# Optimization experiments

Hardware: AMD Instinct MI355X
Metric: run time of the kernel (lower is better)

## Reference

```python
import jax, jax.numpy as jnp
import numpy as np

NUM_QUBITS = 6
NUM_LAYER = 3
INPUT_SIZE = 512
NUM_ANGLES = NUM_LAYER * (4 * NUM_QUBITS - 1)  # 69
BATCH = 65536


def _apply_1q(state, U, wire):
    # state: [B, 2,2,2,2,2,2]; U: [B,2,2] complex
    axis = 1 + wire
    s = jnp.moveaxis(state, axis, -1)
    shp = s.shape
    s = s.reshape(s.shape[0], -1, 2)
    s = jnp.einsum('bij,bkj->bki', U, s)
    return jnp.moveaxis(s.reshape(shp), -1, axis)


def _apply_2q(state, U, w0, w1):
    # state: [B, 2,...,2]; U: [B,4,4] complex; wires (w0,w1) with w0 the high bit
    s = jnp.moveaxis(state, (1 + w0, 1 + w1), (-2, -1))
    shp = s.shape
    s = s.reshape(s.shape[0], -1, 4)
    s = jnp.einsum('bij,bkj->bki', U, s)
    return jnp.moveaxis(s.reshape(shp), (-2, -1), (1 + w0, 1 + w1))


def _rxx_mat(theta):
    c = jnp.cos(theta / 2).astype(jnp.complex64)
    s = (-1j * jnp.sin(theta / 2)).astype(jnp.complex64)
    z = jnp.zeros_like(c)
    return jnp.stack([
        jnp.stack([c, z, z, s], -1),
        jnp.stack([z, c, s, z], -1),
        jnp.stack([z, s, c, z], -1),
        jnp.stack([s, z, z, c], -1),
    ], -2)


def _u3_mat(theta, phi, lam):
    # standard U3 gate: [B,2,2]
    ct = jnp.cos(theta / 2).astype(jnp.complex64)
    st = jnp.sin(theta / 2).astype(jnp.complex64)
    e = lambda a: jnp.exp(1j * a.astype(jnp.complex64))
    return jnp.stack([
        jnp.stack([ct, -e(lam) * st], -1),
        jnp.stack([e(phi) * st, e(phi + lam) * ct], -1),
    ], -2)


def _circuit(angles):
    B = angles.shape[0]
    n = NUM_QUBITS
    state = jnp.zeros((B, 2 ** n), jnp.complex64).at[:, 0].set(1.0)
    state = state.reshape((B,) + (2,) * n)
    per_layer = 4 * n - 1
    for lay in range(NUM_LAYER):
        a = angles[:, lay * per_layer:(lay + 1) * per_layer]
        k = 0
        for i in range(n - 1):
            state = _apply_2q(state, _rxx_mat(a[:, k]), i, i + 1)
            k += 1
            state = _apply_1q(state, _u3_mat(a[:, k], a[:, k + 1], a[:, k + 2]), i)
            k += 3
        state = _apply_1q(state, _u3_mat(a[:, k], a[:, k + 1], a[:, k + 2]), n - 1)
    state = state.reshape(B, 2 ** n)
    # return real/imag stacked: [B, 2, 2^n] float32
    return jnp.stack([state.real, state.imag], axis=1).astype(jnp.float32)


def setup_inputs() -> dict:
    key = jax.random.key(0)
    kx, kw, kb = jax.random.split(key, 3)
    x = jax.random.normal(kx, (BATCH, INPUT_SIZE), dtype=jnp.float32)
    W = jax.random.normal(kw, (NUM_ANGLES, INPUT_SIZE), dtype=jnp.float32) / np.sqrt(INPUT_SIZE)
    b = jax.random.normal(kb, (NUM_ANGLES,), dtype=jnp.float32) * 0.01
    return {"x": x, "W": W, "b": b}


def reference(x, W, b):
    angles = x @ W.T + b  # [B, 69]
    return _circuit(angles)
```

## Files before the change

### kernel.cpp

```cpp
#include <hip/hip_runtime.h>

#define NA    69
#define KDIM  512
#define BM    128
#define BK    64
#define GT    256
#define ASTRIDE 132
#define CROWS 256
#define BLK   256
#define LSTRIDE 33

typedef __attribute__((ext_vector_type(8))) short short8v;
typedef __attribute__((ext_vector_type(4))) float f32x4;
typedef __attribute__((ext_vector_type(4))) unsigned short us4;

__device__ __forceinline__ unsigned short bf16_rne(float x) {
    unsigned u = __float_as_uint(x);
    unsigned r = u + 0x7FFF + ((u >> 16) & 1);
    return (unsigned short)(r >> 16);
}

__global__ void w_convert(const float* __restrict__ W,
                          unsigned short* __restrict__ Whf,
                          unsigned short* __restrict__ Wlf)
{
    int tid = blockIdx.x * 256 + threadIdx.x;
    if (tid >= 16 * 5 * 64) return;
    int ksg = tid / 320;
    int rem = tid % 320;
    int nt  = rem / 64;
    int l   = rem % 64;
    int n   = nt * 16 + (l & 15);
    int k   = ksg * 32 + (l >> 4) * 8;
#pragma unroll
    for (int j = 0; j < 8; ++j) {
        float w = (n < NA) ? W[(size_t)n * KDIM + k + j] : 0.f;
        unsigned short h = bf16_rne(w);
        float hf = __uint_as_float((unsigned)h << 16);
        Whf[(size_t)tid * 8 + j] = h;
        Wlf[(size_t)tid * 8 + j] = bf16_rne(w - hf);
    }
}


template<int M0, int M1>
__device__ __forceinline__ void rxx_l(float* sr, float* si, float th) {
    float h = 0.5f * th, c, sn;
    __sincosf(h, &sn, &c);
    constexpr int M = M0 | M1;
#pragma unroll
    for (int j = 0; j < 32; ++j) {
        if (j & M0) continue;
        const int p = j ^ M;
        float ar = sr[j], ai = si[j], br = sr[p], bi = si[p];
        sr[j] = c * ar + sn * bi;
        si[j] = c * ai - sn * br;
        sr[p] = c * br + sn * ai;
        si[p] = c * bi - sn * ar;
    }
}

template<int M>
__device__ __forceinline__ void u3_l(float* sr, float* si,
                                     float th, float ph, float la) {
    float h = 0.5f * th;
    float ct, st, cph, sph, cla, sla;
    __sincosf(h,  &st,  &ct);
    __sincosf(ph, &sph, &cph);
    __sincosf(la, &sla, &cla);
    float cpl = cph * cla - sph * sla;
    float spl = sph * cla + cph * sla;
    float m01r = -cla * st, m01i = -sla * st;
    float m10r =  cph * st, m10i =  sph * st;
    float m11r =  cpl * ct, m11i =  spl * ct;
#pragma unroll
    for (int j = 0; j < 32; ++j) {
        if (j & M) continue;
        const int p = j | M;
        float ar = sr[j], ai = si[j], br = sr[p], bi = si[p];
        sr[j] = ct * ar + m01r * br - m01i * bi;
        si[j] = ct * ai + m01r * bi + m01i * br;
        sr[p] = m10r * ar - m10i * ai + m11r * br - m11i * bi;
        si[p] = m10r * ai + m10i * ar + m11r * bi + m11i * br;
    }
}

__device__ __forceinline__ void rxx01_x(float* sr, float* si, float th) {
    float h = 0.5f * th, c, sn;
    __sincosf(h, &sn, &c);
#pragma unroll
    for (int j = 0; j < 16; ++j) {
        const int p = j + 16;
        float crj = __shfl_xor(sr[p], 32), cij = __shfl_xor(si[p], 32);
        float crp = __shfl_xor(sr[j], 32), cip = __shfl_xor(si[j], 32);
        float aj = sr[j], bj = si[j], ap = sr[p], bp = si[p];
        sr[j] = c * aj + sn * cij;  si[j] = c * bj - sn * crj;
        sr[p] = c * ap + sn * cip;  si[p] = c * bp - sn * crp;
    }
}

__device__ __forceinline__ void u30_x(float* sr, float* si, int par,
                                      float th, float ph, float la) {
    float h = 0.5f * th;
    float ct, st, cph, sph, cla, sla;
    __sincosf(h,  &st,  &ct);
    __sincosf(ph, &sph, &cph);
    __sincosf(la, &sla, &cla);
    float cpl = cph * cla - sph * sla;
    float spl = sph * cla + cph * sla;
    float m01r = -cla * st, m01i = -sla * st;
    float m10r =  cph * st, m10i =  sph * st;
    float m11r =  cpl * ct, m11i =  spl * ct;
    float Ar = par ? m11r : ct,   Ai = par ? m11i : 0.f;
    float Br = par ? m10r : m01r, Bi = par ? m10i : m01i;
#pragma unroll
    for (int j = 0; j < 32; ++j) {
        float cr = __shfl_xor(sr[j], 32), ci = __shfl_xor(si[j], 32);
        float a = sr[j], bb = si[j];
        sr[j] = Ar * a  - Ai * bb + Br * cr - Bi * ci;
        si[j] = Ar * bb + Ai * a  + Br * ci + Bi * cr;
    }
}


__global__ __launch_bounds__(GT, 3) void qrnn_fused3(
    const float* __restrict__ x,
    const unsigned short* __restrict__ Whf, const unsigned short* __restrict__ Wlf,
    const float* __restrict__ b, float* __restrict__ out)
{
    __shared__ __align__(16) char smem[53248];
    unsigned short* Ah = (unsigned short*)smem;
    unsigned short* Al = (unsigned short*)(smem + 16384);
    unsigned short* Bh = (unsigned short*)(smem + 32768);
    unsigned short* Bl = (unsigned short*)(smem + 43008);
    float* as_ = (float*)smem;

    const int t    = threadIdx.x;
    const int lane = t & 63;
    const int wave = t >> 6;
    const int mb   = blockIdx.x * BM;

    f32x4 acc[2][5];
#pragma unroll
    for (int mt = 0; mt < 2; ++mt)
#pragma unroll
        for (int nt = 0; nt < 5; ++nt) acc[mt][nt] = (f32x4){0.f, 0.f, 0.f, 0.f};

    float4 vA[8];
    short8v vBh0, vBl0, vBh1, vBl1, vBh2, vBl2;

#pragma unroll
    for (int q = 0; q < 8; ++q) {
        int f = t + q * GT, row = f >> 4, col4 = f & 15;
        vA[q] = *reinterpret_cast<const float4*>(
            &x[(size_t)(mb + row) * KDIM + col4 * 4]);
    }
    vBh0 = *reinterpret_cast<const short8v*>(Whf + t * 8);
    vBl0 = *reinterpret_cast<const short8v*>(Wlf + t * 8);
    vBh1 = *reinterpret_cast<const short8v*>(Whf + (t + 256) * 8);
    vBl1 = *reinterpret_cast<const short8v*>(Wlf + (t + 256) * 8);
    if (t < 128) {
        vBh2 = *reinterpret_cast<const short8v*>(Whf + (t + 512) * 8);
        vBl2 = *reinterpret_cast<const short8v*>(Wlf + (t + 512) * 8);
    }

#pragma unroll
    for (int c = 0; c < KDIM / BK; ++c) {
#pragma unroll
        for (int q = 0; q < 8; ++q) {
            int f = t + q * GT, row = f >> 4, col4 = f & 15;
            float vals[4] = {vA[q].x, vA[q].y, vA[q].z, vA[q].w};
            us4 h, lo;
#pragma unroll
            for (int j = 0; j < 4; ++j) {
                unsigned u = __float_as_uint(vals[j]);
                h[j] = (unsigned short)(u >> 16);
                float hf = __uint_as_float(u & 0xFFFF0000u);
                lo[j] = bf16_rne(vals[j] - hf);
            }
            int sw   = (col4 >> 1) ^ (row & 7);
            int byte = row * (BK * 2) + sw * 16 + (col4 & 1) * 8;
            *reinterpret_cast<us4*>((char*)Ah + byte) = h;
            *reinterpret_cast<us4*>((char*)Al + byte) = lo;
        }
        *reinterpret_cast<short8v*>(Bh + t * 8) = vBh0;
        *reinterpret_cast<short8v*>(Bl + t * 8) = vBl0;
        *reinterpret_cast<short8v*>(Bh + (t + 256) * 8) = vBh1;
        *reinterpret_cast<short8v*>(Bl + (t + 256) * 8) = vBl1;
        if (t < 128) {
            *reinterpret_cast<short8v*>(Bh + (t + 512) * 8) = vBh2;
            *reinterpret_cast<short8v*>(Bl + (t + 512) * 8) = vBl2;
        }
        if (c + 1 < KDIM / BK) {
#pragma unroll
            for (int q = 0; q < 8; ++q) {
                int f = t + q * GT, row = f >> 4, col4 = f & 15;
                vA[q] = *reinterpret_cast<const float4*>(
                    &x[(size_t)(mb + row) * KDIM + (c + 1) * BK + col4 * 4]);
            }
            size_t base = (size_t)(c + 1) * 5120;
            vBh0 = *reinterpret_cast<const short8v*>(Whf + base + t * 8);
            vBl0 = *reinterpret_cast<const short8v*>(Wlf + base + t * 8);
            vBh1 = *reinterpret_cast<const short8v*>(Whf + base + (t + 256) * 8);
            vBl1 = *reinterpret_cast<const short8v*>(Wlf + base + (t + 256) * 8);
            if (t < 128) {
                vBh2 = *reinterpret_cast<const short8v*>(Whf + base + (t + 512) * 8);
                vBl2 = *reinterpret_cast<const short8v*>(Wlf + base + (t + 512) * 8);
            }
        }
        __syncthreads();

#pragma unroll
        for (int ks = 0; ks < BK / 32; ++ks) {
            short8v ah[2], al[2];
#pragma unroll
            for (int mt = 0; mt < 2; ++mt) {
                int row = wave * 32 + mt * 16 + (lane & 15);
                int c8  = ks * 4 + (lane >> 4);
                int sw  = c8 ^ (row & 7);
                int abyte = row * (BK * 2) + sw * 16;
                ah[mt] = *reinterpret_cast<const short8v*>((char*)Ah + abyte);
                al[mt] = *reinterpret_cast<const short8v*>((char*)Al + abyte);
            }
#pragma unroll
            for (int nt = 0; nt < 5; ++nt) {
                int boff = ((ks * 5 + nt) * 64 + lane) * 8;
                short8v bh = *reinterpret_cast<const short8v*>(Bh + boff);
                short8v bl = *reinterpret_cast<const short8v*>(Bl + boff);
#pragma unroll
                for (int mt = 0; mt < 2; ++mt) {
                    acc[mt][nt] = __builtin_amdgcn_mfma_f32_16x16x32_bf16(ah[mt], bh, acc[mt][nt], 0, 0, 0);
                    acc[mt][nt] = __builtin_amdgcn_mfma_f32_16x16x32_bf16(al[mt], bh, acc[mt][nt], 0, 0, 0);
                    acc[mt][nt] = __builtin_amdgcn_mfma_f32_16x16x32_bf16(ah[mt], bl, acc[mt][nt], 0, 0, 0);
                }
            }
        }
        __syncthreads();
    }

#pragma unroll
    for (int mt = 0; mt < 2; ++mt)
#pragma unroll
        for (int nt = 0; nt < 5; ++nt) {
            int n = nt * 16 + (lane & 15);
            if (n < NA) {
                float bias = b[n];
                int m = wave * 32 + mt * 16 + (lane >> 4) * 4;
                f32x4 v = acc[mt][nt];
#pragma unroll
                for (int j = 0; j < 4; ++j)
                    as_[n * ASTRIDE + m + j] = v[j] + bias;
            }
        }
    __syncthreads();

    const int par = lane >> 5;
    const int rl  = (lane & 31) + wave * 32;

    float sr[32], si[32];
#pragma unroll
    for (int j = 0; j < 32; ++j) { sr[j] = 0.f; si[j] = 0.f; }
    if (par == 0) sr[0] = 1.f;

#define ANG(i) as_[(i) * ASTRIDE + rl]
#pragma unroll 1
    for (int lay = 0; lay < 3; ++lay) {
        const int base = lay * 23;
        rxx01_x(sr, si, ANG(base + 0));
        u30_x  (sr, si, par, ANG(base + 1), ANG(base + 2), ANG(base + 3));
        rxx_l<16, 8>(sr, si, ANG(base + 4));
        u3_l<16>(sr, si, ANG(base + 5),  ANG(base + 6),  ANG(base + 7));
        rxx_l<8, 4>(sr, si, ANG(base + 8));
        u3_l<8>(sr, si, ANG(base + 9),  ANG(base + 10), ANG(base + 11));
        rxx_l<4, 2>(sr, si, ANG(base + 12));
        u3_l<4>(sr, si, ANG(base + 13), ANG(base + 14), ANG(base + 15));
        rxx_l<2, 1>(sr, si, ANG(base + 16));
        u3_l<2>(sr, si, ANG(base + 17), ANG(base + 18), ANG(base + 19));
        u3_l<1>(sr, si, ANG(base + 20), ANG(base + 21), ANG(base + 22));
    }
#undef ANG

    float* o = out + (size_t)(mb + rl) * 128 + par * 32;
#pragma unroll
    for (int q = 0; q < 8; ++q)
        *reinterpret_cast<float4*>(&o[q * 4]) =
            make_float4(sr[q*4], sr[q*4+1], sr[q*4+2], sr[q*4+3]);
#pragma unroll
    for (int q = 0; q < 8; ++q)
        *reinterpret_cast<float4*>(&o[64 + q * 4]) =
            make_float4(si[q*4], si[q*4+1], si[q*4+2], si[q*4+3]);
}


__global__ __launch_bounds__(BLK, 1) void angles_gemm(
    const float* __restrict__ x, const float* __restrict__ W,
    const float* __restrict__ b, float* __restrict__ ang,
    int row_base, int pass_rows)
{
    const int t     = threadIdx.x;
    const int lrow0 = blockIdx.x * BLK;
    __shared__ float xs[BLK * LSTRIDE];
    float acc[NA];
#pragma unroll
    for (int a = 0; a < NA; ++a) acc[a] = b[a];
    for (int kc = 0; kc < KDIM; kc += 32) {
        __syncthreads();
#pragma unroll
        for (int it = 0; it < 8; ++it) {
            int f4 = it * BLK + t;
            int r  = f4 >> 3;
            int kq = f4 & 7;
            float4 v = *reinterpret_cast<const float4*>(
                &x[(size_t)(row_base + lrow0 + r) * KDIM + kc + kq * 4]);
            *reinterpret_cast<float4*>(&xs[r * LSTRIDE + kq * 4]) = v;
        }
        __syncthreads();
        float4 xv[8];
#pragma unroll
        for (int q = 0; q < 8; ++q)
            xv[q] = *reinterpret_cast<const float4*>(&xs[t * LSTRIDE + q * 4]);
#pragma unroll
        for (int a = 0; a < NA; ++a) {
            const float* wa = W + a * KDIM + kc;
            float s = 0.f;
#pragma unroll
            for (int q = 0; q < 8; ++q) {
                s += xv[q].x * wa[q * 4 + 0];
                s += xv[q].y * wa[q * 4 + 1];
                s += xv[q].z * wa[q * 4 + 2];
                s += xv[q].w * wa[q * 4 + 3];
            }
            acc[a] += s;
        }
    }
    const int lrow = lrow0 + t;
#pragma unroll
    for (int a = 0; a < NA; ++a)
        ang[(size_t)a * pass_rows + lrow] = acc[a];
}

__global__ __launch_bounds__(512, 2) void circuit2g(
    const float* __restrict__ ang, float* __restrict__ out,
    int stride, int row_base)
{
    const int t    = threadIdx.x;
    const int lane = t & 63;
    const int wv   = t >> 6;
    const int par  = lane >> 5;
    const int rl   = (lane & 31) + wv * 32;
    const int row0 = blockIdx.x * CROWS;

    __shared__ float as_[NA][CROWS];
    for (int i = t; i < NA * CROWS; i += 512) {
        int a = i >> 8, r = i & 255;
        as_[a][r] = ang[(size_t)a * stride + row0 + r];
    }
    __syncthreads();

    float sr[32], si[32];
#pragma unroll
    for (int j = 0; j < 32; ++j) { sr[j] = 0.f; si[j] = 0.f; }
    if (par == 0) sr[0] = 1.f;

#define ANG(i) as_[(i)][rl]
#pragma unroll 1
    for (int lay = 0; lay < 3; ++lay) {
        const int base = lay * 23;
        rxx01_x(sr, si, ANG(base + 0));
        u30_x  (sr, si, par, ANG(base + 1), ANG(base + 2), ANG(base + 3));
        rxx_l<16, 8>(sr, si, ANG(base + 4));
        u3_l<16>(sr, si, ANG(base + 5),  ANG(base + 6),  ANG(base + 7));
        rxx_l<8, 4>(sr, si, ANG(base + 8));
        u3_l<8>(sr, si, ANG(base + 9),  ANG(base + 10), ANG(base + 11));
        rxx_l<4, 2>(sr, si, ANG(base + 12));
        u3_l<4>(sr, si, ANG(base + 13), ANG(base + 14), ANG(base + 15));
        rxx_l<2, 1>(sr, si, ANG(base + 16));
        u3_l<2>(sr, si, ANG(base + 17), ANG(base + 18), ANG(base + 19));
        u3_l<1>(sr, si, ANG(base + 20), ANG(base + 21), ANG(base + 22));
    }
#undef ANG

    float* o = out + (size_t)(row_base + row0 + rl) * 128 + par * 32;
#pragma unroll
    for (int q = 0; q < 8; ++q)
        *reinterpret_cast<float4*>(&o[q * 4]) =
            make_float4(sr[q*4], sr[q*4+1], sr[q*4+2], sr[q*4+3]);
#pragma unroll
    for (int q = 0; q < 8; ++q)
        *reinterpret_cast<float4*>(&o[64 + q * 4]) =
            make_float4(si[q*4], si[q*4+1], si[q*4+2], si[q*4+3]);
}


extern "C" void kernel_launch(void* const* d_in, const int* in_sizes, int n_in,
                              void* d_out, int out_size, void* d_ws, size_t ws_size,
                              hipStream_t stream) {
    const float* x = (const float*)d_in[0];
    const float* W = (const float*)d_in[1];
    const float* b = (const float*)d_in[2];
    float* out = (float*)d_out;
    const int batch = in_sizes[0] / KDIM;

    const size_t wf_elems = (size_t)16 * 5 * 64 * 8;
    const size_t need     = 2 * wf_elems * 2;

    if (ws_size >= need && (batch % BM) == 0) {
        unsigned short* Whf = (unsigned short*)d_ws;
        unsigned short* Wlf = Whf + wf_elems;
        hipLaunchKernelGGL(w_convert, dim3((16 * 5 * 64 + 255) / 256), dim3(256),
                           0, stream, W, Whf, Wlf);
        hipLaunchKernelGGL(qrnn_fused3, dim3(batch / BM), dim3(GT), 0, stream,
                           x, Whf, Wlf, b, out);
        return;
    }

    float* ws = (float*)d_ws;
    size_t max_rows = ws_size / ((size_t)NA * sizeof(float));
    int rows_per_pass = (int)((max_rows / CROWS) * CROWS);
    if (rows_per_pass > batch) rows_per_pass = batch;
    if (rows_per_pass < CROWS) return;
    for (int r0 = 0; r0 < batch; r0 += rows_per_pass) {
        int pr = batch - r0;
        if (pr > rows_per_pass) pr = rows_per_pass;
        hipLaunchKernelGGL(angles_gemm, dim3(pr / BLK), dim3(BLK), 0, stream,
                           x, W, b, ws, r0, pr);
        hipLaunchKernelGGL(circuit2g, dim3(pr / CROWS), dim3(512), 0, stream,
                           ws, out, pr, r0);
    }
}
```

Before: 65.65 us.

## Halve fused GEMM+circuit row tile to 64 and raise occupancy

The fused kernel now processes 64 rows per block instead of 128, with one MFMA row tile per wave instead of two. This shrinks LDS use and register pressure and raises launch bounds to 4 blocks per CU, giving twice as many blocks. The cost is that only two of the four waves run the circuit simulation, so half the threads sit idle in that phase. Each W fragment is also reloaded per 64 rows rather than per 128, doubling B traffic.

Result: slower. 138.5 us (+110.9%).

```diff
diff --git a/kernel.cpp b/kernel.cpp
--- a/kernel.cpp
+++ b/kernel.cpp
@@ -2,10 +2,10 @@
 
 #define NA    69
 #define KDIM  512
-#define BM    128
+#define BM    64
 #define BK    64
 #define GT    256
-#define ASTRIDE 132
+#define ASTR  68
 #define CROWS 256
 #define BLK   256
 #define LSTRIDE 33
@@ -44,7 +44,7 @@
 
 
 template<int M0, int M1>
-__device__ __forceinline__ void rxx_l(float* sr, float* si, float th) {
+__device__ __forceinline__ void rxx_l32(float* sr, float* si, float th) {
     float h = 0.5f * th, c, sn;
     __sincosf(h, &sn, &c);
     constexpr int M = M0 | M1;
@@ -61,8 +61,8 @@
 }
 
 template<int M>
-__device__ __forceinline__ void u3_l(float* sr, float* si,
-                                     float th, float ph, float la) {
+__device__ __forceinline__ void u3_l32(float* sr, float* si,
+                                       float th, float ph, float la) {
     float h = 0.5f * th;
     float ct, st, cph, sph, cla, sla;
     __sincosf(h,  &st,  &ct);
@@ -85,7 +85,7 @@
     }
 }
 
-__device__ __forceinline__ void rxx01_x(float* sr, float* si, float th) {
+__device__ __forceinline__ void rxx01_x32(float* sr, float* si, float th) {
     float h = 0.5f * th, c, sn;
     __sincosf(h, &sn, &c);
 #pragma unroll
@@ -99,8 +99,8 @@
     }
 }
 
-__device__ __forceinline__ void u30_x(float* sr, float* si, int par,
-                                      float th, float ph, float la) {
+__device__ __forceinline__ void u30_x32(float* sr, float* si, int par,
+                                        float th, float ph, float la) {
     float h = 0.5f * th;
     float ct, st, cph, sph, cla, sla;
     __sincosf(h,  &st,  &ct);
@@ -123,16 +123,16 @@
 }
 
 
-__global__ __launch_bounds__(GT, 3) void qrnn_fused3(
+__global__ __launch_bounds__(GT, 4) void qrnn_fused5(
     const float* __restrict__ x,
     const unsigned short* __restrict__ Whf, const unsigned short* __restrict__ Wlf,
     const float* __restrict__ b, float* __restrict__ out)
 {
-    __shared__ __align__(16) char smem[53248];
+    __shared__ __align__(16) char smem[36864];
     unsigned short* Ah = (unsigned short*)smem;
-    unsigned short* Al = (unsigned short*)(smem + 16384);
-    unsigned short* Bh = (unsigned short*)(smem + 32768);
-    unsigned short* Bl = (unsigned short*)(smem + 43008);
+    unsigned short* Al = (unsigned short*)(smem + 8192);
+    unsigned short* Bh = (unsigned short*)(smem + 16384);
+    unsigned short* Bl = (unsigned short*)(smem + 26624);
     float* as_ = (float*)smem;
 
     const int t    = threadIdx.x;
@@ -140,17 +140,15 @@
     const int wave = t >> 6;
     const int mb   = blockIdx.x * BM;
 
-    f32x4 acc[2][5];
-#pragma unroll
-    for (int mt = 0; mt < 2; ++mt)
-#pragma unroll
-        for (int nt = 0; nt < 5; ++nt) acc[mt][nt] = (f32x4){0.f, 0.f, 0.f, 0.f};
-
-    float4 vA[8];
+    f32x4 acc[5];
+#pragma unroll
+    for (int nt = 0; nt < 5; ++nt) acc[nt] = (f32x4){0.f, 0.f, 0.f, 0.f};
+
+    float4 vA[4];
     short8v vBh0, vBl0, vBh1, vBl1, vBh2, vBl2;
 
 #pragma unroll
-    for (int q = 0; q < 8; ++q) {
+    for (int q = 0; q < 4; ++q) {
         int f = t + q * GT, row = f >> 4, col4 = f & 15;
         vA[q] = *reinterpret_cast<const float4*>(
             &x[(size_t)(mb + row) * KDIM + col4 * 4]);
@@ -167,7 +165,7 @@
 #pragma unroll
     for (int c = 0; c < KDIM / BK; ++c) {
 #pragma unroll
-        for (int q = 0; q < 8; ++q) {
+        for (int q = 0; q < 4; ++q) {
             int f = t + q * GT, row = f >> 4, col4 = f & 15;
             float vals[4] = {vA[q].x, vA[q].y, vA[q].z, vA[q].w};
             us4 h, lo;
@@ -193,7 +191,7 @@
         }
         if (c + 1 < KDIM / BK) {
 #pragma unroll
-            for (int q = 0; q < 8; ++q) {
+            for (int q = 0; q < 4; ++q) {
                 int f = t + q * GT, row = f >> 4, col4 = f & 15;
                 vA[q] = *reinterpret_cast<const float4*>(
                     &x[(size_t)(mb + row) * KDIM + (c + 1) * BK + col4 * 4]);
@@ -212,83 +210,76 @@
 
 #pragma unroll
         for (int ks = 0; ks < BK / 32; ++ks) {
-            short8v ah[2], al[2];
-#pragma unroll
-            for (int mt = 0; mt < 2; ++mt) {
-                int row = wave * 32 + mt * 16 + (lane & 15);
-                int c8  = ks * 4 + (lane >> 4);
-                int sw  = c8 ^ (row & 7);
-                int abyte = row * (BK * 2) + sw * 16;
-                ah[mt] = *reinterpret_cast<const short8v*>((char*)Ah + abyte);
-                al[mt] = *reinterpret_cast<const short8v*>((char*)Al + abyte);
-            }
+            int row = wave * 16 + (lane & 15);
+            int c8  = ks * 4 + (lane >> 4);
+            int sw  = c8 ^ (row & 7);
+            int abyte = row * (BK * 2) + sw * 16;
+            short8v ah = *reinterpret_cast<const short8v*>((char*)Ah + abyte);
+            short8v al = *reinterpret_cast<const short8v*>((char*)Al + abyte);
 #pragma unroll
             for (int nt = 0; nt < 5; ++nt) {
                 int boff = ((ks * 5 + nt) * 64 + lane) * 8;
                 short8v bh = *reinterpret_cast<const short8v*>(Bh + boff);
                 short8v bl = *reinterpret_cast<const short8v*>(Bl + boff);
-#pragma unroll
-                for (int mt = 0; mt < 2; ++mt) {
-                    acc[mt][nt] = __builtin_amdgcn_mfma_f32_16x16x32_bf16(ah[mt], bh, acc[mt][nt], 0, 0, 0);
-                    acc[mt][nt] = __builtin_amdgcn_mfma_f32_16x16x32_bf16(al[mt], bh, acc[mt][nt], 0, 0, 0);
-                    acc[mt][nt] = __builtin_amdgcn_mfma_f32_16x16x32_bf16(ah[mt], bl, acc[mt][nt], 0, 0, 0);
-                }
+                acc[nt] = __builtin_amdgcn_mfma_f32_16x16x32_bf16(ah, bh, acc[nt], 0, 0, 0);
+                acc[nt] = __builtin_amdgcn_mfma_f32_16x16x32_bf16(al, bh, acc[nt], 0, 0, 0);
+                acc[nt] = __builtin_amdgcn_mfma_f32_16x16x32_bf16(ah, bl, acc[nt], 0, 0, 0);
             }
         }
         __syncthreads();
     }
 
 #pragma unroll
-    for (int mt = 0; mt < 2; ++mt)
-#pragma unroll
-        for (int nt = 0; nt < 5; ++nt) {
-            int n = nt * 16 + (lane & 15);
-            if (n < NA) {
-                float bias = b[n];
-                int m = wave * 32 + mt * 16 + (lane >> 4) * 4;
-                f32x4 v = acc[mt][nt];
-#pragma unroll
-                for (int j = 0; j < 4; ++j)
-                    as_[n * ASTRIDE + m + j] = v[j] + bias;
-            }
-        }
+    for (int nt = 0; nt < 5; ++nt) {
+        int n = nt * 16 + (lane & 15);
+        if (n < NA) {
+            float bias = b[n];
+            int m0 = wave * 16 + (lane >> 4) * 4;
+            f32x4 v = acc[nt];
+            float4 o = make_float4(v[0] + bias, v[1] + bias,
+                                   v[2] + bias, v[3] + bias);
+            *reinterpret_cast<float4*>(&as_[n * ASTR + m0]) = o;
+        }
+    }
     __syncthreads();
 
-    const int par = lane >> 5;
-    const int rl  = (lane & 31) + wave * 32;
-
-    float sr[32], si[32];
-#pragma unroll
-    for (int j = 0; j < 32; ++j) { sr[j] = 0.f; si[j] = 0.f; }
-    if (par == 0) sr[0] = 1.f;
-
-#define ANG(i) as_[(i) * ASTRIDE + rl]
+    if (wave < 2) {
+        const int par = lane >> 5;
+        const int rl  = (lane & 31) + wave * 32;
+
+        float sr[32], si[32];
+#pragma unroll
+        for (int j = 0; j < 32; ++j) { sr[j] = 0.f; si[j] = 0.f; }
+        if (par == 0) sr[0] = 1.f;
+
+#define ANG(i) as_[(i) * ASTR + rl]
 #pragma unroll 1
-    for (int lay = 0; lay < 3; ++lay) {
-        const int base = lay * 23;
-        rxx01_x(sr, si, ANG(base + 0));
-        u30_x  (sr, si, par, ANG(base + 1), ANG(base + 2), ANG(base + 3));
-        rxx_l<16, 8>(sr, si, ANG(base + 4));
-        u3_l<16>(sr, si, ANG(base + 5),  ANG(base + 6),  ANG(base + 7));
-        rxx_l<8, 4>(sr, si, ANG(base + 8));
-        u3_l<8>(sr, si, ANG(base + 9),  ANG(base + 10), ANG(base + 11));
-        rxx_l<4, 2>(sr, si, ANG(base + 12));
-        u3_l<4>(sr, si, ANG(base + 13), ANG(base + 14), ANG(base + 15));
-        rxx_l<2, 1>(sr, si, ANG(base + 16));
-        u3_l<2>(sr, si, ANG(base + 17), ANG(base + 18), ANG(base + 19));
-        u3_l<1>(sr, si, ANG(base + 20), ANG(base + 21), ANG(base + 22));
-    }
+        for (int lay = 0; lay < 3; ++lay) {
+            const int base = lay * 23;
+            rxx01_x32(sr, si, ANG(base + 0));
+            u30_x32  (sr, si, par, ANG(base + 1), ANG(base + 2), ANG(base + 3));
+            rxx_l32<16, 8>(sr, si, ANG(base + 4));
+            u3_l32<16>(sr, si, ANG(base + 5),  ANG(base + 6),  ANG(base + 7));
+            rxx_l32<8, 4>(sr, si, ANG(base + 8));
+            u3_l32<8>(sr, si, ANG(base + 9),  ANG(base + 10), ANG(base + 11));
+            rxx_l32<4, 2>(sr, si, ANG(base + 12));
+            u3_l32<4>(sr, si, ANG(base + 13), ANG(base + 14), ANG(base + 15));
+            rxx_l32<2, 1>(sr, si, ANG(base + 16));
+            u3_l32<2>(sr, si, ANG(base + 17), ANG(base + 18), ANG(base + 19));
+            u3_l32<1>(sr, si, ANG(base + 20), ANG(base + 21), ANG(base + 22));
+        }
 #undef ANG
 
-    float* o = out + (size_t)(mb + rl) * 128 + par * 32;
-#pragma unroll
-    for (int q = 0; q < 8; ++q)
-        *reinterpret_cast<float4*>(&o[q * 4]) =
-            make_float4(sr[q*4], sr[q*4+1], sr[q*4+2], sr[q*4+3]);
-#pragma unroll
-    for (int q = 0; q < 8; ++q)
-        *reinterpret_cast<float4*>(&o[64 + q * 4]) =
-            make_float4(si[q*4], si[q*4+1], si[q*4+2], si[q*4+3]);
+        float* o = out + (size_t)(mb + rl) * 128 + par * 32;
+#pragma unroll
+        for (int s = 0; s < 8; ++s)
+            *reinterpret_cast<float4*>(&o[s * 4]) =
+                make_float4(sr[s*4], sr[s*4+1], sr[s*4+2], sr[s*4+3]);
+#pragma unroll
+        for (int s = 0; s < 8; ++s)
+            *reinterpret_cast<float4*>(&o[64 + s * 4]) =
+                make_float4(si[s*4], si[s*4+1], si[s*4+2], si[s*4+3]);
+    }
 }
 
 
@@ -366,29 +357,29 @@
 #pragma unroll 1
     for (int lay = 0; lay < 3; ++lay) {
         const int base = lay * 23;
-        rxx01_x(sr, si, ANG(base + 0));
-        u30_x  (sr, si, par, ANG(base + 1), ANG(base + 2), ANG(base + 3));
-        rxx_l<16, 8>(sr, si, ANG(base + 4));
-        u3_l<16>(sr, si, ANG(base + 5),  ANG(base + 6),  ANG(base + 7));
-        rxx_l<8, 4>(sr, si, ANG(base + 8));
-        u3_l<8>(sr, si, ANG(base + 9),  ANG(base + 10), ANG(base + 11));
-        rxx_l<4, 2>(sr, si, ANG(base + 12));
-        u3_l<4>(sr, si, ANG(base + 13), ANG(base + 14), ANG(base + 15));
-        rxx_l<2, 1>(sr, si, ANG(base + 16));
-        u3_l<2>(sr, si, ANG(base + 17), ANG(base + 18), ANG(base + 19));
-        u3_l<1>(sr, si, ANG(base + 20), ANG(base + 21), ANG(base + 22));
+        rxx01_x32(sr, si, ANG(base + 0));
+        u30_x32  (sr, si, par, ANG(base + 1), ANG(base + 2), ANG(base + 3));
+        rxx_l32<16, 8>(sr, si, ANG(base + 4));
+        u3_l32<16>(sr, si, ANG(base + 5),  ANG(base + 6),  ANG(base + 7));
+        rxx_l32<8, 4>(sr, si, ANG(base + 8));
+        u3_l32<8>(sr, si, ANG(base + 9),  ANG(base + 10), ANG(base + 11));
+        rxx_l32<4, 2>(sr, si, ANG(base + 12));
+        u3_l32<4>(sr, si, ANG(base + 13), ANG(base + 14), ANG(base + 15));
+        rxx_l32<2, 1>(sr, si, ANG(base + 16));
+        u3_l32<2>(sr, si, ANG(base + 17), ANG(base + 18), ANG(base + 19));
+        u3_l32<1>(sr, si, ANG(base + 20), ANG(base + 21), ANG(base + 22));
     }
 #undef ANG
 
     float* o = out + (size_t)(row_base + row0 + rl) * 128 + par * 32;
 #pragma unroll
-    for (int q = 0; q < 8; ++q)
-        *reinterpret_cast<float4*>(&o[q * 4]) =
-            make_float4(sr[q*4], sr[q*4+1], sr[q*4+2], sr[q*4+3]);
-#pragma unroll
-    for (int q = 0; q < 8; ++q)
-        *reinterpret_cast<float4*>(&o[64 + q * 4]) =
-            make_float4(si[q*4], si[q*4+1], si[q*4+2], si[q*4+3]);
+    for (int s = 0; s < 8; ++s)
+        *reinterpret_cast<float4*>(&o[s * 4]) =
+            make_float4(sr[s*4], sr[s*4+1], sr[s*4+2], sr[s*4+3]);
+#pragma unroll
+    for (int s = 0; s < 8; ++s)
+        *reinterpret_cast<float4*>(&o[64 + s * 4]) =
+            make_float4(si[s*4], si[s*4+1], si[s*4+2], si[s*4+3]);
 }
 
 
@@ -409,7 +400,7 @@
         unsigned short* Wlf = Whf + wf_elems;
         hipLaunchKernelGGL(w_convert, dim3((16 * 5 * 64 + 255) / 256), dim3(256),
                            0, stream, W, Whf, Wlf);
-        hipLaunchKernelGGL(qrnn_fused3, dim3(batch / BM), dim3(GT), 0, stream,
+        hipLaunchKernelGGL(qrnn_fused5, dim3(batch / BM), dim3(GT), 0, stream,
                            x, Whf, Wlf, b, out);
         return;
     }
```
